# Performance work log

Measured on AMD Instinct MI355X. Metric: run time of the kernel, lower is better.

Reference implementation:

```python
import jax, jax.numpy as jnp
import numpy as np

B, C, H, W = 32, 256, 56, 56
NUM_ITER = 5

# Row-major upper-triangular (incl. diagonal) flat indices, matching
# torch.ones(C, C).triu().view(-1).nonzero() in the original triuvec.
_r, _c = np.triu_indices(C)
TRIU_IDX = jnp.asarray(_r * C + _c)


def setup_inputs() -> dict:
    key = jax.random.key(0)
    x = jax.random.normal(key, (B, C, H, W), dtype=jnp.float32)
    return {"x": x}


def _cov_pool(x):
    # x: (b, c, h, w) -> sigma = x_n @ ((1/n) I - (1/n^2) J) @ x_n^T : (b, c, c)
    b, c, h, w = x.shape
    n = h * w
    xn = x.reshape(b, c, n)
    s = xn.sum(axis=2)  # (b, c) = x_n @ ones
    gram = jnp.einsum('bcn,bdn->bcd', xn, xn)  # (b, c, c)
    return gram / n - jnp.einsum('bc,bd->bcd', s, s) / (n * n)


def _newton_schulz_sqrt(x, num_iter):
    # x: (b, m, m) SPD; returns approx matrix square root, scaled by sqrt(trace).
    b, m, _ = x.shape
    eye = jnp.eye(m, dtype=x.dtype)
    x_trace = jnp.trace(x, axis1=1, axis2=2)[:, None, None]  # (b, 1, 1)
    a = x / x_trace
    i3 = 3.0 * eye  # broadcasts over batch
    # iteration 0
    b2 = 0.5 * (i3 - a)
    yi = a @ b2
    zi = b2

    def body(carry, _):
        yi, zi = carry
        b2 = 0.5 * (i3 - zi @ yi)
        return (yi @ b2, b2 @ zi), None

    (yi, zi), _ = jax.lax.scan(body, (yi, zi), None, length=num_iter - 1)
    return yi * jnp.sqrt(x_trace)


def _triuvec(x):
    # (b, c, c) -> (b, c*(c+1)//2), row-major upper triangle incl. diagonal
    b, c, _ = x.shape
    return x.reshape(b, c * c)[:, TRIU_IDX]


def reference(x) -> jnp.ndarray:
    cov = _cov_pool(x)
    y = _newton_schulz_sqrt(cov, NUM_ITER)
    return _triuvec(y)
```

## Files before the change

kernel.cpp:

```cpp
#include <hip/hip_runtime.h>
#include <hip/hip_bf16.h>
#include <math.h>

#define BATCH 32
#define C 256
#define HW 3136
#define OUTROW 32896
#define KSPLIT 7
#define KCHUNK 448
#define KC32 98
#define KCG 49
#define SLAB 16384
#define HALF 8192


typedef __bf16 b8v __attribute__((ext_vector_type(8)));
typedef float  f4v __attribute__((ext_vector_type(4)));
typedef unsigned short u16x8 __attribute__((ext_vector_type(8)));

__device__ __forceinline__ unsigned short f2bf(float f) {
    union { float f; unsigned u; } v; v.f = f;
    unsigned r = v.u + 0x7FFFu + ((v.u >> 16) & 1u);
    return (unsigned short)(r >> 16);
}
__device__ __forceinline__ float bf2f(unsigned short h) {
    union { unsigned u; float f; } v; v.u = ((unsigned)h) << 16; return v.f;
}
__device__ __forceinline__ void split2(float x, unsigned short& h, unsigned short& l) {
    h = f2bf(x);
    l = f2bf(x - bf2f(h));
}

__device__ __forceinline__ float wave_sum(float v) {
    for (int o = 32; o; o >>= 1) v += __shfl_down(v, o, 64);
    return v;
}

__global__ __launch_bounds__(256) void k_prep(const float* __restrict__ x,
                                              unsigned short* __restrict__ X,
                                              float* __restrict__ psum,
                                              float* __restrict__ qsum) {
    const int blk = blockIdx.x;
    const int b = blk / KCG;
    const int g = blk - b * KCG;
    const int kc0 = g * 2;
    const int t = threadIdx.x;
    const int lane4 = t & 3;
    const int rowoff = t >> 2;
    const int ko = lane4 * 8;

    const float* xb = x + (size_t)b * C * HW + (size_t)kc0 * 32 + ko;
    unsigned short* s0 = X + (size_t)(b * KC32 + kc0) * SLAB + ko;
    unsigned short* s1 = s0 + SLAB;
    float* ps = psum + (size_t)blk * 256;
    float* qs = qsum + (size_t)blk * 256;

#pragma unroll
    for (int it = 0; it < 4; ++it) {
        const int row = it * 64 + rowoff;
        const float* src = xb + (size_t)row * HW;
        float4 v0 = *(const float4*)(src);
        float4 v1 = *(const float4*)(src + 4);
        float4 v2 = *(const float4*)(src + 32);
        float4 v3 = *(const float4*)(src + 36);
        float va[8] = { v0.x, v0.y, v0.z, v0.w, v1.x, v1.y, v1.z, v1.w };
        float vb[8] = { v2.x, v2.y, v2.z, v2.w, v3.x, v3.y, v3.z, v3.w };
        unsigned short ha[8], la[8], hb[8], lb[8];
        float s = 0.f, q = 0.f;
#pragma unroll
        for (int j = 0; j < 8; ++j) {
            split2(va[j], ha[j], la[j]);
            split2(vb[j], hb[j], lb[j]);
            s += va[j] + vb[j];
            q = fmaf(va[j], va[j], q);
            q = fmaf(vb[j], vb[j], q);
        }
        *(u16x8*)(s0 + row * 32) = *(u16x8*)ha;
        *(u16x8*)(s0 + HALF + row * 32) = *(u16x8*)la;
        *(u16x8*)(s1 + row * 32) = *(u16x8*)hb;
        *(u16x8*)(s1 + HALF + row * 32) = *(u16x8*)lb;
        s += __shfl_xor(s, 1, 64);
        s += __shfl_xor(s, 2, 64);
        q += __shfl_xor(q, 1, 64);
        q += __shfl_xor(q, 2, 64);
        if (lane4 == 0) { ps[row] = s; qs[row] = q; }
    }
}

__global__ __launch_bounds__(256) void k_tr(const float* __restrict__ psum,
                                            const float* __restrict__ qsum,
                                            float* __restrict__ sbuf,
                                            float* __restrict__ trbuf,
                                            float* __restrict__ strbuf) {
    const int b = blockIdx.x, t = threadIdx.x;
    const float* ps = psum + (size_t)b * KCG * 256 + t;
    const float* qs = qsum + (size_t)b * KCG * 256 + t;
    float s = 0.f, q = 0.f;
#pragma unroll 7
    for (int g = 0; g < KCG; ++g) {
        s += ps[(size_t)g * 256];
        q += qs[(size_t)g * 256];
    }
    sbuf[b * C + t] = s;
    const float invn = 1.f / (float)HW, invn2 = invn * invn;
    float v = q * invn - s * s * invn2;
    v = wave_sum(v);
    __shared__ float red[4];
    if ((t & 63) == 0) red[t >> 6] = v;
    __syncthreads();
    if (t == 0) {
        float tr = red[0] + red[1] + red[2] + red[3];
        trbuf[b] = tr;
        strbuf[b] = sqrtf(tr);
    }
}

__global__ __launch_bounds__(64, 1) void k_gram_split(
    const unsigned short* __restrict__ X, float* __restrict__ part) {
    const int bid = blockIdx.x;
    const int x8 = bid & 7;
    const int t8 = bid >> 3;
    const int pairIdx = t8 % 10;
    const int g = (t8 / 10) * 8 + x8;
    const int b = g & 31;
    const int z = g >> 5;

    int p = pairIdx, tm = 0, rem = 4;
    while (p >= rem) { p -= rem; ++tm; --rem; }
    const int tn = tm + p;

    const int lane = threadIdx.x & 63;
    const int q = lane >> 4, r = lane & 15;
    const int kc0 = z * (KCHUNK / 32);
    const size_t matb = (size_t)b * KC32 * SLAB;

    int oA[4], oB[4];
#pragma unroll
    for (int i = 0; i < 4; ++i) {
        oA[i] = (tm * 64 + i * 16 + r) * 32 + q * 8;
        oB[i] = (tn * 64 + i * 16 + r) * 32 + q * 8;
    }

    f4v acc[4][4] = {};
    b8v fAh[2][4], fAl[2][4], fBh[2][4], fBl[2][4];
#define LDG(buf, kc)                                                     \
    do {                                                                 \
        const size_t sb = matb + (size_t)(kc0 + (kc)) * SLAB;            \
        for (int i = 0; i < 4; ++i) {                                    \
            fAh[buf][i] = *(const b8v*)(X + sb + oA[i]);                 \
            fAl[buf][i] = *(const b8v*)(X + sb + HALF + oA[i]);          \
            fBh[buf][i] = *(const b8v*)(X + sb + oB[i]);                 \
            fBl[buf][i] = *(const b8v*)(X + sb + HALF + oB[i]);          \
        }                                                                \
    } while (0)

    LDG(0, 0);
#pragma unroll
    for (int kc = 0; kc < KCHUNK / 32; ++kc) {
        const int cb = kc & 1, nb = cb ^ 1;
        if (kc < KCHUNK / 32 - 1) LDG(nb, kc + 1);
#pragma unroll
        for (int i = 0; i < 4; ++i)
#pragma unroll
            for (int j = 0; j < 4; ++j) {
                acc[i][j] = __builtin_amdgcn_mfma_f32_16x16x32_bf16(fAh[cb][i], fBh[cb][j], acc[i][j], 0, 0, 0);
                acc[i][j] = __builtin_amdgcn_mfma_f32_16x16x32_bf16(fAh[cb][i], fBl[cb][j], acc[i][j], 0, 0, 0);
                acc[i][j] = __builtin_amdgcn_mfma_f32_16x16x32_bf16(fAl[cb][i], fBh[cb][j], acc[i][j], 0, 0, 0);
            }
    }
#undef LDG

    float* pt = part + (((size_t)pairIdx * BATCH + b) * KSPLIT + z) * 4096;
#pragma unroll
    for (int i = 0; i < 4; ++i)
#pragma unroll
        for (int j = 0; j < 4; ++j)
#pragma unroll
            for (int reg = 0; reg < 4; ++reg) {
                int row = i * 16 + q * 4 + reg;
                int col = j * 16 + r;
                pt[row * 64 + col] = acc[i][j][reg];
            }
}

__global__ __launch_bounds__(256) void k_reduce(
    const float* __restrict__ part, const float* __restrict__ sbuf,
    const float* __restrict__ trbuf,
    unsigned short* __restrict__ A, unsigned short* __restrict__ Z) {
    const int b = blockIdx.y;
    int p = blockIdx.x, tm = 0, rem = 4;
    while (p >= rem) { p -= rem; ++tm; --rem; }
    const int tn = tm + p;

    const float* pb = part + ((size_t)blockIdx.x * BATCH + b) * KSPLIT * 4096;
    const int t = threadIdx.x;
    const int row = t >> 2, c0 = (t & 3) * 16;

    float s[16];
#pragma unroll
    for (int u = 0; u < 16; ++u) s[u] = 0.f;
    for (int sp = 0; sp < KSPLIT; ++sp) {
        const float* q4 = pb + sp * 4096 + row * 64 + c0;
#pragma unroll
        for (int u4 = 0; u4 < 4; ++u4) {
            float4 v = *(const float4*)(q4 + u4 * 4);
            s[u4 * 4 + 0] += v.x; s[u4 * 4 + 1] += v.y;
            s[u4 * 4 + 2] += v.z; s[u4 * 4 + 3] += v.w;
        }
    }

    const float invn = 1.f / (float)HW, invn2 = invn * invn;
    const float tr = trbuf[b];
    const int gi = tm * 64 + row;
    const float si = sbuf[b * C + gi];
    const size_t mb = (size_t)b * 8 * SLAB;

    __shared__ unsigned short tAh[64][66], tAl[64][66], tZh[64][66], tZl[64][66];
    unsigned short vAh[16], vAl[16], vZh[16], vZl[16];
#pragma unroll
    for (int u = 0; u < 16; ++u) {
        int gj = tn * 64 + c0 + u;
        float sj = sbuf[b * C + gj];
        float a = (s[u] * invn - si * sj * invn2) / tr;
        split2(a, vAh[u], vAl[u]);
        float zv = ((gi == gj) ? 1.5f : 0.f) - 0.5f * a;
        split2(zv, vZh[u], vZl[u]);
        tAh[row][c0 + u] = vAh[u]; tAl[row][c0 + u] = vAl[u];
        tZh[row][c0 + u] = vZh[u]; tZl[row][c0 + u] = vZl[u];
    }
#pragma unroll
    for (int u4 = 0; u4 < 4; ++u4) {
        const int col0 = tn * 64 + c0 + u4 * 4;
        const size_t off = mb + (size_t)(col0 >> 5) * SLAB + (size_t)gi * 32 + (col0 & 31);
        *(ushort4*)&A[off] = *(ushort4*)&vAh[u4 * 4];
        *(ushort4*)&A[off + HALF] = *(ushort4*)&vAl[u4 * 4];
        *(ushort4*)&Z[off] = *(ushort4*)&vZh[u4 * 4];
        *(ushort4*)&Z[off + HALF] = *(ushort4*)&vZl[u4 * 4];
    }
    if (tm != tn) {
        __syncthreads();
        const int mr = t >> 2, mc0 = (t & 3) * 16;
        const int gim = tn * 64 + mr;
        unsigned short wAh[16], wAl[16], wZh[16], wZl[16];
#pragma unroll
        for (int u = 0; u < 16; ++u) {
            wAh[u] = tAh[mc0 + u][mr]; wAl[u] = tAl[mc0 + u][mr];
            wZh[u] = tZh[mc0 + u][mr]; wZl[u] = tZl[mc0 + u][mr];
        }
#pragma unroll
        for (int u4 = 0; u4 < 4; ++u4) {
            const int col0 = tm * 64 + mc0 + u4 * 4;
            const size_t off = mb + (size_t)(col0 >> 5) * SLAB + (size_t)gim * 32 + (col0 & 31);
            *(ushort4*)&A[off] = *(ushort4*)&wAh[u4 * 4];
            *(ushort4*)&A[off + HALF] = *(ushort4*)&wAl[u4 * 4];
            *(ushort4*)&Z[off] = *(ushort4*)&wZh[u4 * 4];
            *(ushort4*)&Z[off + HALF] = *(ushort4*)&wZl[u4 * 4];
        }
    }
}

__device__ __forceinline__ void wave_gemm32(
    const unsigned short* __restrict__ A, const unsigned short* __restrict__ B,
    int rowA, int rowB, f4v acc[2][2]) {
    const int lane = threadIdx.x & 63;
    const int q = lane >> 4, r = lane & 15;
    int oA[2], oB[2];
#pragma unroll
    for (int i = 0; i < 2; ++i) {
        oA[i] = (rowA + i * 16 + r) * 32 + q * 8;
        oB[i] = (rowB + i * 16 + r) * 32 + q * 8;
    }
    b8v fAh[2][2], fAl[2][2], fBh[2][2], fBl[2][2];
#define LD(buf, kc)                                              \
    do {                                                         \
        const size_t sb = (size_t)(kc) * SLAB;                   \
        for (int i = 0; i < 2; ++i) {                            \
            fAh[buf][i] = *(const b8v*)(A + sb + oA[i]);         \
            fAl[buf][i] = *(const b8v*)(A + sb + HALF + oA[i]);  \
            fBh[buf][i] = *(const b8v*)(B + sb + oB[i]);         \
            fBl[buf][i] = *(const b8v*)(B + sb + HALF + oB[i]);  \
        }                                                        \
    } while (0)

    LD(0, 0);
#pragma unroll
    for (int kc = 0; kc < 8; ++kc) {
        const int cb = kc & 1, nb = cb ^ 1;
        if (kc < 7) LD(nb, kc + 1);
#pragma unroll
        for (int i = 0; i < 2; ++i)
#pragma unroll
            for (int j = 0; j < 2; ++j) {
                acc[i][j] = __builtin_amdgcn_mfma_f32_16x16x32_bf16(fAh[cb][i], fBh[cb][j], acc[i][j], 0, 0, 0);
                acc[i][j] = __builtin_amdgcn_mfma_f32_16x16x32_bf16(fAh[cb][i], fBl[cb][j], acc[i][j], 0, 0, 0);
                acc[i][j] = __builtin_amdgcn_mfma_f32_16x16x32_bf16(fAl[cb][i], fBh[cb][j], acc[i][j], 0, 0, 0);
            }
    }
#undef LD
}

__device__ __forceinline__ void store_tile32(
    unsigned short* __restrict__ D, int tm, int tn, const f4v acc[2][2], bool modeT) {
    const int lane = threadIdx.x & 63, q = lane >> 4, r = lane & 15;
#pragma unroll
    for (int i = 0; i < 2; ++i)
#pragma unroll
        for (int j = 0; j < 2; ++j) {
            const int gj = tn * 32 + j * 16 + r;
            const size_t cbase = (size_t)(gj >> 5) * SLAB + (gj & 31);
#pragma unroll
            for (int reg = 0; reg < 4; ++reg) {
                const int gi = tm * 32 + i * 16 + q * 4 + reg;
                float v = acc[i][j][reg];
                if (modeT) v = ((gi == gj) ? 1.5f : 0.f) - 0.5f * v;
                unsigned short h, l;
                split2(v, h, l);
                D[cbase + (size_t)gi * 32] = h;
                D[cbase + HALF + (size_t)gi * 32] = l;
            }
        }
}

template <int MODE>
__global__ __launch_bounds__(64, 1) void k_t64(
    const unsigned short* __restrict__ A, const unsigned short* __restrict__ B,
    unsigned short* __restrict__ D, float* __restrict__ outF,
    const float* __restrict__ strbuf) {
    const int bid = blockIdx.x;
    const int x8 = bid & 7;
    const int w = bid >> 3;
    int b, tm = 0, tn = 0;
    if (MODE == 2) {
        b = x8 + 8 * (w / 36);
        int p = w % 36, rem = 8;
        while (p >= rem) { p -= rem; ++tm; --rem; }
        tn = tm + p;
    } else {
        b = x8 + 8 * (w >> 6);
        const int tile = w & 63;
        tm = tile >> 3; tn = tile & 7;
    }
    const size_t mo = (size_t)b * 8 * SLAB;
    f4v acc[2][2] = {};
    wave_gemm32(A + mo, B + mo, tm * 32, tn * 32, acc);

    if (MODE == 2) {
        const int lane = threadIdx.x & 63, q = lane >> 4, r = lane & 15;
        const float sc = strbuf[b];
#pragma unroll
        for (int i = 0; i < 2; ++i)
#pragma unroll
            for (int j = 0; j < 2; ++j) {
                const int gj = tn * 32 + j * 16 + r;
#pragma unroll
                for (int reg = 0; reg < 4; ++reg) {
                    const int gi = tm * 32 + i * 16 + q * 4 + reg;
                    if (gj >= gi)
                        outF[(size_t)b * OUTROW + (size_t)(gi * C - (gi * (gi - 1)) / 2) +
                             (gj - gi)] = acc[i][j][reg] * sc;
                }
            }
    } else {
        store_tile32(D + mo, tm, tn, acc, MODE == 1);
    }
}

__global__ __launch_bounds__(64, 1) void k_yz64(
    const unsigned short* __restrict__ Y, const unsigned short* __restrict__ T,
    const unsigned short* __restrict__ Z,
    unsigned short* __restrict__ Yn, unsigned short* __restrict__ Zn) {
    const int bid = blockIdx.x;
    const int x8 = bid & 7;
    const int w = bid >> 3;
    const int zz = w >> 8;
    const int ww = w & 255;
    const int b = x8 + 8 * (ww >> 6);
    const int tile = ww & 63;
    const int tm = tile >> 3, tn = tile & 7;

    const unsigned short* Am = zz ? T : Y;
    const unsigned short* Bm = zz ? Z : T;
    unsigned short* Dm = zz ? Zn : Yn;

    const size_t mo = (size_t)b * 8 * SLAB;
    f4v acc[2][2] = {};
    wave_gemm32(Am + mo, Bm + mo, tm * 32, tn * 32, acc);
    store_tile32(Dm + mo, tm, tn, acc, false);
}

extern "C" void kernel_launch(void* const* d_in, const int* in_sizes, int n_in,
                              void* d_out, int out_size, void* d_ws, size_t ws_size,
                              hipStream_t stream) {
    const float* x = (const float*)d_in[0];
    float* out = (float*)d_out;

    unsigned short* W = (unsigned short*)d_ws;
    const size_t XS = (size_t)BATCH * KC32 * SLAB;
    const size_t MS = (size_t)BATCH * 8 * SLAB;
    unsigned short* X = W;
    float* sbuf = (float*)(X + XS);
    float* trbuf = sbuf + BATCH * C;
    float* strbuf = trbuf + BATCH;
    unsigned short* P = (unsigned short*)(strbuf + BATCH);
    unsigned short* PA = P + 0 * MS;
    unsigned short* PB = P + 1 * MS;
    unsigned short* PC = P + 2 * MS;
    unsigned short* PD = P + 3 * MS;
    unsigned short* PE = P + 4 * MS;
    float* part = (float*)PC;
    float* psum = (float*)PA;
    float* qsum = psum + (size_t)BATCH * KCG * 256;

    k_prep<<<dim3(BATCH * KCG), 256, 0, stream>>>(x, X, psum, qsum);
    k_tr<<<dim3(BATCH), 256, 0, stream>>>(psum, qsum, sbuf, trbuf, strbuf);
    k_gram_split<<<dim3(10 * BATCH * KSPLIT), 64, 0, stream>>>(X, part);
    k_reduce<<<dim3(10, BATCH), 256, 0, stream>>>(part, sbuf, trbuf, PA, PB);

    dim3 g2048(2048);
    k_t64<0><<<g2048, 64, 0, stream>>>(PA, PB, PC, nullptr, strbuf);
    k_t64<1><<<g2048, 64, 0, stream>>>(PB, PC, PD, nullptr, strbuf);
    k_yz64<<<dim3(4096), 64, 0, stream>>>(PC, PD, PB, PA, PE);
    k_t64<1><<<g2048, 64, 0, stream>>>(PE, PA, PB, nullptr, strbuf);
    k_yz64<<<dim3(4096), 64, 0, stream>>>(PA, PB, PE, PC, PD);
    k_t64<1><<<g2048, 64, 0, stream>>>(PD, PC, PA, nullptr, strbuf);
    k_yz64<<<dim3(4096), 64, 0, stream>>>(PC, PA, PD, PB, PE);
    k_t64<1><<<g2048, 64, 0, stream>>>(PE, PB, PC, nullptr, strbuf);
    k_t64<2><<<dim3(1152), 64, 0, stream>>>(PB, PC, nullptr, out, strbuf);
}
```

Measured before the change: 349.1 us.

## Fold trace reduction into k_reduce and remap k_prep to per-row slab threads

```diff
diff --git a/kernel.cpp b/kernel.cpp
--- a/kernel.cpp
+++ b/kernel.cpp
@@ -9,7 +9,7 @@
 #define KSPLIT 7
 #define KCHUNK 448
 #define KC32 98
-#define KCG 49
+#define G7 14
 #define SLAB 16384
 #define HALF 8192
 
@@ -36,82 +36,55 @@
     return v;
 }
 
-__global__ __launch_bounds__(256) void k_prep(const float* __restrict__ x,
-                                              unsigned short* __restrict__ X,
-                                              float* __restrict__ psum,
-                                              float* __restrict__ qsum) {
-    const int blk = blockIdx.x;
-    const int b = blk / KCG;
-    const int g = blk - b * KCG;
-    const int kc0 = g * 2;
+__global__ __launch_bounds__(256, 2) void k_prep(const float* __restrict__ x,
+                                                 unsigned short* __restrict__ X,
+                                                 float* __restrict__ psum,
+                                                 float* __restrict__ qsum) {
+    const int bid = blockIdx.x;
+    const int quad = bid & 3;
+    const int bg = bid >> 2;
+    const int b = bg / G7;
+    const int g = bg - b * G7;
     const int t = threadIdx.x;
-    const int lane4 = t & 3;
-    const int rowoff = t >> 2;
-    const int ko = lane4 * 8;
-
-    const float* xb = x + (size_t)b * C * HW + (size_t)kc0 * 32 + ko;
-    unsigned short* s0 = X + (size_t)(b * KC32 + kc0) * SLAB + ko;
-    unsigned short* s1 = s0 + SLAB;
-    float* ps = psum + (size_t)blk * 256;
-    float* qs = qsum + (size_t)blk * 256;
-
-#pragma unroll
-    for (int it = 0; it < 4; ++it) {
-        const int row = it * 64 + rowoff;
-        const float* src = xb + (size_t)row * HW;
-        float4 v0 = *(const float4*)(src);
-        float4 v1 = *(const float4*)(src + 4);
-        float4 v2 = *(const float4*)(src + 32);
-        float4 v3 = *(const float4*)(src + 36);
-        float va[8] = { v0.x, v0.y, v0.z, v0.w, v1.x, v1.y, v1.z, v1.w };
-        float vb[8] = { v2.x, v2.y, v2.z, v2.w, v3.x, v3.y, v3.z, v3.w };
-        unsigned short ha[8], la[8], hb[8], lb[8];
-        float s = 0.f, q = 0.f;
-#pragma unroll
-        for (int j = 0; j < 8; ++j) {
-            split2(va[j], ha[j], la[j]);
-            split2(vb[j], hb[j], lb[j]);
-            s += va[j] + vb[j];
-            q = fmaf(va[j], va[j], q);
-            q = fmaf(vb[j], vb[j], q);
+    if (t >= 252) return;
+    const int j = t % 7;
+    const int rbase = t / 7;
+    const int kc = g * 7 + j;
+
+    const float* xb = x + (size_t)b * C * HW + (size_t)kc * 32;
+    unsigned short* sl = X + (size_t)(b * KC32 + kc) * SLAB;
+    float* ps = psum + ((size_t)b * KC32 + kc) * 256;
+    float* qs = qsum + ((size_t)b * KC32 + kc) * 256;
+
+#pragma unroll
+    for (int p = 0; p < 2; ++p) {
+        const int row = quad * 64 + p * 36 + rbase;
+        if (row < quad * 64 + 64) {
+            const float* src = xb + (size_t)row * HW;
+            float4 v[8];
+#pragma unroll
+            for (int u = 0; u < 8; ++u) v[u] = *(const float4*)(src + u * 4);
+            unsigned short h[32], l[32];
+            float s = 0.f, q = 0.f;
+#pragma unroll
+            for (int u = 0; u < 8; ++u) {
+                float f0 = v[u].x, f1 = v[u].y, f2 = v[u].z, f3 = v[u].w;
+                split2(f0, h[u * 4 + 0], l[u * 4 + 0]);
+                split2(f1, h[u * 4 + 1], l[u * 4 + 1]);
+                split2(f2, h[u * 4 + 2], l[u * 4 + 2]);
+                split2(f3, h[u * 4 + 3], l[u * 4 + 3]);
+                s += f0 + f1 + f2 + f3;
+                q = fmaf(f0, f0, q); q = fmaf(f1, f1, q);
+                q = fmaf(f2, f2, q); q = fmaf(f3, f3, q);
+            }
+#pragma unroll
+            for (int u = 0; u < 4; ++u) {
+                *(u16x8*)(sl + (size_t)row * 32 + u * 8) = *(u16x8*)&h[u * 8];
+                *(u16x8*)(sl + HALF + (size_t)row * 32 + u * 8) = *(u16x8*)&l[u * 8];
+            }
+            ps[row] = s;
+            qs[row] = q;
         }
-        *(u16x8*)(s0 + row * 32) = *(u16x8*)ha;
-        *(u16x8*)(s0 + HALF + row * 32) = *(u16x8*)la;
-        *(u16x8*)(s1 + row * 32) = *(u16x8*)hb;
-        *(u16x8*)(s1 + HALF + row * 32) = *(u16x8*)lb;
-        s += __shfl_xor(s, 1, 64);
-        s += __shfl_xor(s, 2, 64);
-        q += __shfl_xor(q, 1, 64);
-        q += __shfl_xor(q, 2, 64);
-        if (lane4 == 0) { ps[row] = s; qs[row] = q; }
-    }
-}
-
-__global__ __launch_bounds__(256) void k_tr(const float* __restrict__ psum,
-                                            const float* __restrict__ qsum,
-                                            float* __restrict__ sbuf,
-                                            float* __restrict__ trbuf,
-                                            float* __restrict__ strbuf) {
-    const int b = blockIdx.x, t = threadIdx.x;
-    const float* ps = psum + (size_t)b * KCG * 256 + t;
-    const float* qs = qsum + (size_t)b * KCG * 256 + t;
-    float s = 0.f, q = 0.f;
-#pragma unroll 7
-    for (int g = 0; g < KCG; ++g) {
-        s += ps[(size_t)g * 256];
-        q += qs[(size_t)g * 256];
-    }
-    sbuf[b * C + t] = s;
-    const float invn = 1.f / (float)HW, invn2 = invn * invn;
-    float v = q * invn - s * s * invn2;
-    v = wave_sum(v);
-    __shared__ float red[4];
-    if ((t & 63) == 0) red[t >> 6] = v;
-    __syncthreads();
-    if (t == 0) {
-        float tr = red[0] + red[1] + red[2] + red[3];
-        trbuf[b] = tr;
-        strbuf[b] = sqrtf(tr);
     }
 }
 
@@ -184,16 +157,36 @@
 }
 
 __global__ __launch_bounds__(256) void k_reduce(
-    const float* __restrict__ part, const float* __restrict__ sbuf,
-    const float* __restrict__ trbuf,
-    unsigned short* __restrict__ A, unsigned short* __restrict__ Z) {
+    const float* __restrict__ part, const float* __restrict__ psum,
+    const float* __restrict__ qsum,
+    unsigned short* __restrict__ A, unsigned short* __restrict__ Z,
+    float* __restrict__ strbuf) {
     const int b = blockIdx.y;
     int p = blockIdx.x, tm = 0, rem = 4;
     while (p >= rem) { p -= rem; ++tm; --rem; }
     const int tn = tm + p;
+    const int t = threadIdx.x;
+
+    const float* ps = psum + (size_t)b * KC32 * 256 + t;
+    const float* qs = qsum + (size_t)b * KC32 * 256 + t;
+    float s0 = 0.f, q0 = 0.f;
+#pragma unroll 7
+    for (int kc = 0; kc < KC32; ++kc) {
+        s0 += ps[(size_t)kc * 256];
+        q0 += qs[(size_t)kc * 256];
+    }
+    __shared__ float ssum[256];
+    __shared__ float red[4];
+    ssum[t] = s0;
+    const float invn = 1.f / (float)HW, invn2 = invn * invn;
+    float v = q0 * invn - s0 * s0 * invn2;
+    v = wave_sum(v);
+    if ((t & 63) == 0) red[t >> 6] = v;
+    __syncthreads();
+    const float tr = red[0] + red[1] + red[2] + red[3];
+    if (blockIdx.x == 0 && t == 0) strbuf[b] = sqrtf(tr);
 
     const float* pb = part + ((size_t)blockIdx.x * BATCH + b) * KSPLIT * 4096;
-    const int t = threadIdx.x;
     const int row = t >> 2, c0 = (t & 3) * 16;
 
     float s[16];
@@ -203,16 +196,14 @@
         const float* q4 = pb + sp * 4096 + row * 64 + c0;
 #pragma unroll
         for (int u4 = 0; u4 < 4; ++u4) {
-            float4 v = *(const float4*)(q4 + u4 * 4);
-            s[u4 * 4 + 0] += v.x; s[u4 * 4 + 1] += v.y;
-            s[u4 * 4 + 2] += v.z; s[u4 * 4 + 3] += v.w;
+            float4 w = *(const float4*)(q4 + u4 * 4);
+            s[u4 * 4 + 0] += w.x; s[u4 * 4 + 1] += w.y;
+            s[u4 * 4 + 2] += w.z; s[u4 * 4 + 3] += w.w;
         }
     }
 
-    const float invn = 1.f / (float)HW, invn2 = invn * invn;
-    const float tr = trbuf[b];
     const int gi = tm * 64 + row;
-    const float si = sbuf[b * C + gi];
+    const float si = ssum[gi];
     const size_t mb = (size_t)b * 8 * SLAB;
 
     __shared__ unsigned short tAh[64][66], tAl[64][66], tZh[64][66], tZl[64][66];
@@ -220,7 +211,7 @@
 #pragma unroll
     for (int u = 0; u < 16; ++u) {
         int gj = tn * 64 + c0 + u;
-        float sj = sbuf[b * C + gj];
+        float sj = ssum[gj];
         float a = (s[u] * invn - si * sj * invn2) / tr;
         split2(a, vAh[u], vAl[u]);
         float zv = ((gi == gj) ? 1.5f : 0.f) - 0.5f * a;
@@ -398,9 +389,7 @@
     const size_t XS = (size_t)BATCH * KC32 * SLAB;
     const size_t MS = (size_t)BATCH * 8 * SLAB;
     unsigned short* X = W;
-    float* sbuf = (float*)(X + XS);
-    float* trbuf = sbuf + BATCH * C;
-    float* strbuf = trbuf + BATCH;
+    float* strbuf = (float*)(X + XS);
     unsigned short* P = (unsigned short*)(strbuf + BATCH);
     unsigned short* PA = P + 0 * MS;
     unsigned short* PB = P + 1 * MS;
@@ -408,13 +397,13 @@
     unsigned short* PD = P + 3 * MS;
     unsigned short* PE = P + 4 * MS;
     float* part = (float*)PC;
-    float* psum = (float*)PA;
-    float* qsum = psum + (size_t)BATCH * KCG * 256;
-
-    k_prep<<<dim3(BATCH * KCG), 256, 0, stream>>>(x, X, psum, qsum);
-    k_tr<<<dim3(BATCH), 256, 0, stream>>>(psum, qsum, sbuf, trbuf, strbuf);
+    unsigned short* partEnd = PC + (size_t)2 * 10 * BATCH * KSPLIT * 4096;
+    float* psum = (float*)partEnd;
+    float* qsum = psum + (size_t)BATCH * KC32 * 256;
+
+    k_prep<<<dim3(BATCH * G7 * 4), 256, 0, stream>>>(x, X, psum, qsum);
     k_gram_split<<<dim3(10 * BATCH * KSPLIT), 64, 0, stream>>>(X, part);
-    k_reduce<<<dim3(10, BATCH), 256, 0, stream>>>(part, sbuf, trbuf, PA, PB);
+    k_reduce<<<dim3(10, BATCH), 256, 0, stream>>>(part, psum, qsum, PA, PB, strbuf);
 
     dim3 g2048(2048);
     k_t64<0><<<g2048, 64, 0, stream>>>(PA, PB, PC, nullptr, strbuf);
```

Measured after the change: 362.1 us. +3.7%, slower.
